# Performance work log

Hardware: AMD Instinct MI355X
Metric: run time of the kernel (lower is better)

The kernel has to match this reference:

```python
import jax, jax.numpy as jnp
import numpy as np

EPS = 1e-8

def elu_feature_map(x):
    return jax.nn.elu(x) + 1.0

def setup_inputs() -> dict:
    key = jax.random.key(0)
    ks = jax.random.split(key, 5)
    B, S, D = 2, 4096, 1024
    scale = 1.0 / np.sqrt(D).astype(np.float32)
    x = jax.random.normal(ks[0], (B, S, D), dtype=jnp.float32)
    Wq = jax.random.normal(ks[1], (D, D), dtype=jnp.float32) * scale
    Wk = jax.random.normal(ks[2], (D, D), dtype=jnp.float32) * scale
    Wv = jax.random.normal(ks[3], (D, D), dtype=jnp.float32) * scale
    Wo = jax.random.normal(ks[4], (D, D), dtype=jnp.float32) * scale
    return {"x": x, "Wq": Wq, "Wk": Wk, "Wv": Wv, "Wo": Wo}

def reference(x, Wq, Wk, Wv, Wo):
    B, S, D = x.shape
    H = 16
    Dh = D // H
    # projections (nn.Linear with no bias: x @ W.T)
    def proj(W):
        return (x @ W.T).reshape(B, S, H, Dh)
    q = elu_feature_map(proj(Wq))  # [B,S,H,Dh]
    k = elu_feature_map(proj(Wk))
    v = proj(Wv)
    # scan over sequence: carry running kv_sum [B,H,Dh,Dh] and k_sum [B,H,Dh]
    q_t = jnp.moveaxis(q, 1, 0)  # [S,B,H,Dh]
    k_t = jnp.moveaxis(k, 1, 0)
    v_t = jnp.moveaxis(v, 1, 0)

    def step(carry, qkv):
        kv_sum, k_sum = carry
        q_i, k_i, v_i = qkv  # each [B,H,Dh]
        kv_sum = kv_sum + jnp.einsum('bhd,bhe->bhde', k_i, v_i)
        k_sum = k_sum + k_i
        num = jnp.einsum('bhd,bhde->bhe', q_i, kv_sum)
        den = jnp.sum(q_i * k_sum, axis=-1, keepdims=True)
        out_i = num / (den + EPS)
        return (kv_sum, k_sum), out_i

    kv0 = jnp.zeros((B, H, Dh, Dh), dtype=x.dtype)
    ks0 = jnp.zeros((B, H, Dh), dtype=x.dtype)
    _, out = jax.lax.scan(step, (kv0, ks0), (q_t, k_t, v_t))  # out: [S,B,H,Dh]
    out = jnp.moveaxis(out, 0, 1).reshape(B, S, D)
    return out @ Wo.T
```

## Files before the change

kernel.cpp:

```cpp
#include <hip/hip_runtime.h>
#include <math.h>


#define EPSF 1e-8f

typedef unsigned short u16;
typedef unsigned int   u32;
typedef __attribute__((ext_vector_type(8))) short short8v;
typedef __attribute__((ext_vector_type(4))) float f32x4;

__device__ __forceinline__ float elu1(float x){ return x > 0.f ? x + 1.f : __expf(x); }
__device__ __forceinline__ u16 f2bf(float f){
    union{float f; u32 i;} c; c.f = f;
    u32 i = c.i + 0x7FFFu + ((c.i >> 16) & 1u);
    return (u16)(i >> 16);
}
__device__ __forceinline__ float bf2f(u16 v){ union{u32 i; float f;} c; c.i = (u32)v << 16; return c.f; }
__device__ __forceinline__ float bflo(u32 v){ union{u32 i; float f;} c; c.i = v << 16; return c.f; }
__device__ __forceinline__ float bfhi(u32 v){ union{u32 i; float f;} c; c.i = v & 0xffff0000u; return c.f; }
__device__ __forceinline__ void f4a(float4 v, float* a){ a[0]=v.x; a[1]=v.y; a[2]=v.z; a[3]=v.w; }

__device__ __forceinline__ void gload16(const void* g, void* l){
    __builtin_amdgcn_global_load_lds((const __attribute__((address_space(1))) u32*)g,
                                     (__attribute__((address_space(3))) u32*)l, 16, 0, 0);
}

__global__ __launch_bounds__(256) void k_cast5(
    const float* __restrict__ x,  const float* __restrict__ wq,
    const float* __restrict__ wk, const float* __restrict__ wv,
    const float* __restrict__ wo,
    u16* __restrict__ xb, u16* __restrict__ wcat, u16* __restrict__ wob)
{
    size_t i8 = ((size_t)blockIdx.x * 256 + threadIdx.x) * 8;
    const float* s; u16* d; size_t off;
    if      (i8 <  8388608) { s = x;  d = xb;            off = i8; }
    else if (i8 <  9437184) { s = wq; d = wcat;          off = i8 - 8388608; }
    else if (i8 < 10485760) { s = wk; d = wcat + 1048576; off = i8 - 9437184; }
    else if (i8 < 11534336) { s = wv; d = wcat + 2097152; off = i8 - 10485760; }
    else                    { s = wo; d = wob;           off = i8 - 11534336; }
    float4 a = *(const float4*)&s[off];
    float4 b = *(const float4*)&s[off + 4];
    uint4 p;
    p.x = (u32)f2bf(a.x) | ((u32)f2bf(a.y) << 16);
    p.y = (u32)f2bf(a.z) | ((u32)f2bf(a.w) << 16);
    p.z = (u32)f2bf(b.x) | ((u32)f2bf(b.y) << 16);
    p.w = (u32)f2bf(b.z) | ((u32)f2bf(b.w) << 16);
    *(uint4*)&d[off] = p;
}

__global__ __launch_bounds__(256, 3) void k_gemm6(
    const u16* __restrict__ Ag, const u16* __restrict__ Wg, u16* __restrict__ C)
{
    __shared__ __align__(16) char dsm[49152];
    const int bid = blockIdx.x;
    const int nid = (bid & 7) * 96 + (bid >> 3);
    const int bx  = nid / 24;
    const int by  = nid % 24;
    const int m0  = bx * 256;
    const int n0  = by * 128;

    const int tid = threadIdx.x;
    const int l   = tid & 63;
    const int wid = tid >> 6;
    const int wm  = wid >> 1;
    const int wn  = wid & 1;
    const int li  = l & 15;
    const int kgi = l >> 4;

    const int ra0 = wm*128 + li;
    const int offA0 = (ra0 >> 1)*128 + (((((ra0 & 1) << 2) | kgi) ^ ((ra0 >> 1) & 7)) << 4);
    const int rb0 = wn*64 + li;
    const int offB0 = (rb0 >> 1)*128 + (((((rb0 & 1) << 2) | kgi) ^ ((rb0 >> 1) & 7)) << 4);

    const int sx   = (l & 7) ^ (l >> 3);
    const int rowb = 2*(wid*8 + (l >> 3)) + (sx >> 2);
    const int skg  = (sx & 3) * 8;
    const u16* srcA = Ag + (size_t)(m0 + rowb) * 1024 + skg;
    const u16* srcB = Wg + (size_t)(n0 + rowb) * 1024 + skg;

    f32x4 acc[8][4];
    #pragma unroll
    for (int m = 0; m < 8; ++m)
        #pragma unroll
        for (int n = 0; n < 4; ++n) acc[m][n] = (f32x4){0.f, 0.f, 0.f, 0.f};

    #define ST6(BUF, T) { \
        char* ab = dsm + (BUF)*24576; \
        char* bb = dsm + (BUF)*24576 + 16384; \
        _Pragma("unroll") for (int j = 0; j < 4; ++j) \
            gload16(srcA + (size_t)j*65536 + (T)*32, ab + j*4096 + wid*1024); \
        _Pragma("unroll") for (int j = 0; j < 2; ++j) \
            gload16(srcB + (size_t)j*65536 + (T)*32, bb + j*4096 + wid*1024); }

    ST6(0, 0);
    asm volatile("s_waitcnt vmcnt(0)" ::: "memory");
    __builtin_amdgcn_s_barrier();

    #pragma unroll 1
    for (int t = 0; t < 32; ++t) {
        const int cur = t & 1;
        if (t < 31) ST6(cur ^ 1, t + 1);
        const char* Ab = dsm + cur*24576;
        const char* Bb = dsm + cur*24576 + 16384;
        short8v bfr[4];
        #pragma unroll
        for (int n = 0; n < 4; ++n) bfr[n] = *(const short8v*)(Bb + offB0 + n*1024);
        __builtin_amdgcn_s_setprio(1);
        #pragma unroll
        for (int m = 0; m < 8; ++m) {
            short8v afr = *(const short8v*)(Ab + offA0 + m*1024);
            #pragma unroll
            for (int n = 0; n < 4; ++n)
                acc[m][n] = __builtin_amdgcn_mfma_f32_16x16x32_bf16(afr, bfr[n], acc[m][n], 0, 0, 0);
        }
        __builtin_amdgcn_s_setprio(0);
        asm volatile("s_waitcnt vmcnt(0)" ::: "memory");
        __builtin_amdgcn_s_barrier();
    }
    #undef ST6

    const int matrix = by >> 3;
    const bool do_elu = matrix < 2;
    u16* outp = C + (size_t)matrix * 8388608;
    const int r0 = m0 + wm*128 + kgi*4;
    const int c0 = (by & 7)*128 + wn*64 + li;
    #pragma unroll
    for (int m = 0; m < 8; ++m)
        #pragma unroll
        for (int n = 0; n < 4; ++n)
            #pragma unroll
            for (int r = 0; r < 4; ++r) {
                float v = acc[m][n][r];
                if (do_elu) v = elu1(v);
                outp[(size_t)(r0 + m*16 + r) * 1024 + c0 + n*16] = f2bf(v);
            }
}

#define AOFF(BUF,KH) ((BUF)*49152 + (KH)*8192)
#define BOFF(BUF,KH) ((BUF)*49152 + 16384 + (KH)*16384)

#define ST(BUF, KT, KH) { \
    gload16(Ag + (size_t)(m0 + sRow)*1024 + (KT)*64 + (KH)*32 + sKg, dsm + AOFF(BUF,KH) + wvv*1024); \
    gload16(Wg + (size_t)(n0 + sRow)*1024 + (KT)*64 + (KH)*32 + sKg, dsm + BOFF(BUF,KH) + wvv*1024); \
    gload16(Wg + (size_t)(n0 + 128 + sRow)*1024 + (KT)*64 + (KH)*32 + sKg, dsm + BOFF(BUF,KH) + 8192 + wvv*1024); }

#define PH(BUF, KH, STCODE, CNT) { \
    short8v a[4], b[4]; \
    const char* Ab = dsm + AOFF(BUF,KH); \
    const char* Bb = dsm + BOFF(BUF,KH); \
    _Pragma("unroll") for (int m = 0; m < 4; ++m) a[m] = *(const short8v*)(Ab + offA[m]); \
    _Pragma("unroll") for (int n = 0; n < 4; ++n) b[n] = *(const short8v*)(Bb + offB[n]); \
    STCODE; \
    __builtin_amdgcn_s_setprio(1); \
    _Pragma("unroll") for (int m = 0; m < 4; ++m) \
        _Pragma("unroll") for (int n = 0; n < 4; ++n) \
            acc[m][n] = __builtin_amdgcn_mfma_f32_16x16x32_bf16(a[m], b[n], acc[m][n], 0, 0, 0); \
    __builtin_amdgcn_s_setprio(0); \
    asm volatile("s_waitcnt vmcnt(" #CNT ")" ::: "memory"); \
    __builtin_amdgcn_s_barrier(); }

template<int NBY>
__global__ __launch_bounds__(512, 2) void k_gemm5(
    const u16* __restrict__ Ag, const u16* __restrict__ Wg, float* __restrict__ Cv)
{
    extern __shared__ char dsm[];
    const int nid = (blockIdx.x & 7) * ((64 * NBY) >> 3) + (blockIdx.x >> 3);
    const int bx  = nid / NBY;
    const int by  = nid % NBY;
    const int m0  = bx * 128;
    const int n0  = by * 256;

    const int tid = threadIdx.x;
    const int l   = tid & 63;
    const int wid = tid >> 6;
    const int wm  = wid >> 2;
    const int wn  = wid & 3;
    const int li  = l & 15;
    const int kgi = l >> 4;

    int offA[4], offB[4];
    #pragma unroll
    for (int m = 0; m < 4; ++m) {
        int ra = wm*64 + m*16 + li;
        offA[m] = (ra >> 1)*128 + (((((ra & 1) << 2) | kgi) ^ ((ra >> 1) & 7)) << 4);
        int rb = wn*64 + m*16 + li;
        offB[m] = (rb >> 1)*128 + (((((rb & 1) << 2) | kgi) ^ ((rb >> 1) & 7)) << 4);
    }
    const int wvv  = wid;
    const int sx   = (l & 7) ^ (l >> 3);
    const int sRow = 2*(wvv*8 + (l >> 3)) + (sx >> 2);
    const int sKg  = (sx & 3) * 8;

    f32x4 acc[4][4];
    #pragma unroll
    for (int m = 0; m < 4; ++m)
        #pragma unroll
        for (int n = 0; n < 4; ++n) acc[m][n] = (f32x4){0.f, 0.f, 0.f, 0.f};

    ST(0, 0, 0); ST(0, 0, 1); ST(1, 1, 0);
    asm volatile("s_waitcnt vmcnt(6)" ::: "memory");
    __builtin_amdgcn_s_barrier();

    #pragma unroll 1
    for (int it = 0; it < 7; ++it) {
        const int T = it * 2;
        PH(0, 0, ST(1, T+1, 1), 6);
        PH(0, 1, ST(0, T+2, 0), 6);
        PH(1, 0, ST(0, T+2, 1), 6);
        PH(1, 1, ST(1, T+3, 0), 6);
    }
    PH(0, 0, ST(1, 15, 1), 6);
    PH(0, 1, {}, 3);
    PH(1, 0, {}, 0);
    {
        short8v a[4], b[4];
        const char* Ab = dsm + AOFF(1,1);
        const char* Bb = dsm + BOFF(1,1);
        #pragma unroll
        for (int m = 0; m < 4; ++m) a[m] = *(const short8v*)(Ab + offA[m]);
        #pragma unroll
        for (int n = 0; n < 4; ++n) b[n] = *(const short8v*)(Bb + offB[n]);
        #pragma unroll
        for (int m = 0; m < 4; ++m)
            #pragma unroll
            for (int n = 0; n < 4; ++n)
                acc[m][n] = __builtin_amdgcn_mfma_f32_16x16x32_bf16(a[m], b[n], acc[m][n], 0, 0, 0);
    }

    const int r0 = m0 + wm*64 + (l >> 4) * 4;
    const int c0 = n0 + wn*64 + li;
    #pragma unroll
    for (int m = 0; m < 4; ++m)
        #pragma unroll
        for (int n = 0; n < 4; ++n)
            #pragma unroll
            for (int r = 0; r < 4; ++r)
                Cv[(size_t)(r0 + m*16 + r) * 1024 + c0 + n*16] = acc[m][n][r];
}

__global__ __launch_bounds__(256) void k_chunksums(
    const u16* __restrict__ Kg, const u16* __restrict__ Vg,
    u16* __restrict__ CKVb, float* __restrict__ CKS)
{
    const int tid = threadIdx.x;
    const int tx = tid & 15, ty = tid >> 4;
    const int c  = blockIdx.x & 63;
    const int bh = blockIdx.x >> 6;
    const int b = bh >> 4, h = bh & 15;
    const int row0 = b * 4096 + c * 64;
    const int col  = h * 64;

    __shared__ float Ks[64][68];
    __shared__ float Vs[64][68];

    #pragma unroll
    for (int r = 0; r < 2; ++r) {
        int idx = tid + r * 256;
        int i = idx >> 3, cg = (idx & 7) << 3;
        uint4 ku = *(const uint4*)&Kg[(size_t)(row0 + i) * 1024 + col + cg];
        uint4 vu = *(const uint4*)&Vg[(size_t)(row0 + i) * 1024 + col + cg];
        Ks[i][cg+0]=bflo(ku.x); Ks[i][cg+1]=bfhi(ku.x);
        Ks[i][cg+2]=bflo(ku.y); Ks[i][cg+3]=bfhi(ku.y);
        Ks[i][cg+4]=bflo(ku.z); Ks[i][cg+5]=bfhi(ku.z);
        Ks[i][cg+6]=bflo(ku.w); Ks[i][cg+7]=bfhi(ku.w);
        Vs[i][cg+0]=bflo(vu.x); Vs[i][cg+1]=bfhi(vu.x);
        Vs[i][cg+2]=bflo(vu.y); Vs[i][cg+3]=bfhi(vu.y);
        Vs[i][cg+4]=bflo(vu.z); Vs[i][cg+5]=bfhi(vu.z);
        Vs[i][cg+6]=bflo(vu.w); Vs[i][cg+7]=bfhi(vu.w);
    }
    __syncthreads();

    float acc[4][4] = {};
    #pragma unroll 8
    for (int i = 0; i < 64; ++i) {
        float kv[4], vv[4];
        f4a(*(const float4*)&Ks[i][ty*4], kv);
        f4a(*(const float4*)&Vs[i][tx*4], vv);
        #pragma unroll
        for (int a = 0; a < 4; ++a)
            #pragma unroll
            for (int e = 0; e < 4; ++e)
                acc[a][e] = fmaf(kv[a], vv[e], acc[a][e]);
    }
    u16* ckv = &CKVb[(size_t)blockIdx.x * 4096];
    #pragma unroll
    for (int e = 0; e < 4; ++e) {
        u32 p0 = (u32)f2bf(acc[0][e]) | ((u32)f2bf(acc[1][e]) << 16);
        u32 p1 = (u32)f2bf(acc[2][e]) | ((u32)f2bf(acc[3][e]) << 16);
        *(uint2*)&ckv[(tx*4 + e) * 64 + ty*4] = make_uint2(p0, p1);
    }

    if (tid < 64) {
        float s = 0.f;
        #pragma unroll 8
        for (int i = 0; i < 64; ++i) s += Ks[i][tid];
        CKS[(size_t)blockIdx.x * 64 + tid] = s;
    }
}

__global__ __launch_bounds__(256) void k_prefix_kv(u16* __restrict__ CKV)
{
    const int bh = blockIdx.x >> 4;
    const int p  = ((blockIdx.x & 15) << 8) + threadIdx.x;
    const size_t base = (size_t)bh * 64 * 4096 + p;
    float acc = 0.f;
    #pragma unroll
    for (int c = 0; c < 64; ++c) {
        float t = bf2f(CKV[base + (size_t)c * 4096]);
        CKV[base + (size_t)c * 4096] = f2bf(acc);
        acc += t;
    }
}

__global__ __launch_bounds__(256) void k_prefix_ks(float* __restrict__ CKS)
{
    const int idx = blockIdx.x * 256 + threadIdx.x;
    const int bh = idx >> 6, d = idx & 63;
    const size_t base = (size_t)bh * 64 * 64 + d;
    float v[64];
    #pragma unroll
    for (int c = 0; c < 64; ++c) v[c] = CKS[base + (size_t)c * 64];
    float acc = 0.f;
    #pragma unroll
    for (int c = 0; c < 64; ++c) { float t = v[c]; CKS[base + (size_t)c * 64] = acc; acc += t; }
}

#define LSTR 72
__global__ __launch_bounds__(256) void k_attn2(
    const u16* __restrict__ Qg, const u16* __restrict__ Kg, const u16* __restrict__ Vg,
    const u16* __restrict__ Stg, const float* __restrict__ KSg, u16* __restrict__ AO)
{
    const int tid = threadIdx.x;
    const int l = tid & 63;
    const int w = tid >> 6;
    const int c  = blockIdx.x & 63;
    const int bh = blockIdx.x >> 6;
    const int row0 = (bh >> 4) * 4096 + c * 64;
    const int col  = (bh & 15) * 64;

    __shared__ __align__(16) u16 Qs [64 * LSTR];
    __shared__ __align__(16) u16 Ks [64 * LSTR];
    __shared__ __align__(16) u16 Vt [64 * LSTR];
    __shared__ __align__(16) u16 Sts[64 * LSTR];
    __shared__ __align__(16) u16 Pl [64 * LSTR];
    __shared__ float ksumF[64];
    __shared__ float invdenL[64];

    #pragma unroll
    for (int r = 0; r < 2; ++r) {
        int idx = tid + r * 256;
        int i = idx >> 3, cg = (idx & 7) << 3;
        *(uint4*)&Qs [i*LSTR + cg] = *(const uint4*)&Qg [(size_t)(row0 + i) * 1024 + col + cg];
        *(uint4*)&Ks [i*LSTR + cg] = *(const uint4*)&Kg [(size_t)(row0 + i) * 1024 + col + cg];
        *(uint4*)&Sts[i*LSTR + cg] = *(const uint4*)&Stg[(size_t)blockIdx.x * 4096 + i * 64 + cg];
        uint4 vu = *(const uint4*)&Vg[(size_t)(row0 + i) * 1024 + col + cg];
        Vt[(cg+0)*LSTR + i] = (u16)(vu.x & 0xffff);
        Vt[(cg+1)*LSTR + i] = (u16)(vu.x >> 16);
        Vt[(cg+2)*LSTR + i] = (u16)(vu.y & 0xffff);
        Vt[(cg+3)*LSTR + i] = (u16)(vu.y >> 16);
        Vt[(cg+4)*LSTR + i] = (u16)(vu.z & 0xffff);
        Vt[(cg+5)*LSTR + i] = (u16)(vu.z >> 16);
        Vt[(cg+6)*LSTR + i] = (u16)(vu.w & 0xffff);
        Vt[(cg+7)*LSTR + i] = (u16)(vu.w >> 16);
    }
    if (tid < 64) ksumF[tid] = KSg[(size_t)blockIdx.x * 64 + tid];
    __syncthreads();

    const int li = l & 15;
    const int lg = l >> 4;
    const int i_row = w * 16 + li;

    short8v bq[2];
    #pragma unroll
    for (int kc = 0; kc < 2; ++kc)
        bq[kc] = *(const short8v*)&Qs[i_row * LSTR + lg*8 + kc*32];

    float den = EPSF;
    #pragma unroll
    for (int mj = 0; mj < 4; ++mj) {
        f32x4 sacc = (f32x4){0.f, 0.f, 0.f, 0.f};
        #pragma unroll
        for (int kc = 0; kc < 2; ++kc) {
            short8v ak = *(const short8v*)&Ks[(mj*16 + li) * LSTR + lg*8 + kc*32];
            sacc = __builtin_amdgcn_mfma_f32_16x16x32_bf16(ak, bq[kc], sacc, 0, 0, 0);
        }
        const int jbase = mj*16 + lg*4;
        float pv[4];
        #pragma unroll
        for (int r = 0; r < 4; ++r) {
            float v = sacc[r];
            v = (jbase + r <= i_row) ? v : 0.f;
            den += v;
            pv[r] = v;
        }
        u32 lo = (u32)f2bf(pv[0]) | ((u32)f2bf(pv[1]) << 16);
        u32 hi = (u32)f2bf(pv[2]) | ((u32)f2bf(pv[3]) << 16);
        *(uint2*)&Pl[i_row * LSTR + jbase] = make_uint2(lo, hi);
    }

    {
        const int d0 = lg * 16;
        uint4 q1 = *(const uint4*)&Qs[i_row * LSTR + d0];
        uint4 q2 = *(const uint4*)&Qs[i_row * LSTR + d0 + 8];
        den += bflo(q1.x)*ksumF[d0+0] + bfhi(q1.x)*ksumF[d0+1]
             + bflo(q1.y)*ksumF[d0+2] + bfhi(q1.y)*ksumF[d0+3]
             + bflo(q1.z)*ksumF[d0+4] + bfhi(q1.z)*ksumF[d0+5]
             + bflo(q1.w)*ksumF[d0+6] + bfhi(q1.w)*ksumF[d0+7]
             + bflo(q2.x)*ksumF[d0+8] + bfhi(q2.x)*ksumF[d0+9]
             + bflo(q2.y)*ksumF[d0+10]+ bfhi(q2.y)*ksumF[d0+11]
             + bflo(q2.z)*ksumF[d0+12]+ bfhi(q2.z)*ksumF[d0+13]
             + bflo(q2.w)*ksumF[d0+14]+ bfhi(q2.w)*ksumF[d0+15];
    }
    den += __shfl_xor(den, 16);
    den += __shfl_xor(den, 32);
    if (l < 16) invdenL[w*16 + l] = 1.f / den;

    f32x4 oacc[4];
    #pragma unroll
    for (int ne = 0; ne < 4; ++ne) oacc[ne] = (f32x4){0.f, 0.f, 0.f, 0.f};
    #pragma unroll
    for (int kc = 0; kc < 2; ++kc) {
        short8v ap = *(const short8v*)&Pl[i_row * LSTR + lg*8 + kc*32];
        short8v aq = bq[kc];
        #pragma unroll
        for (int ne = 0; ne < 4; ++ne) {
            short8v bv = *(const short8v*)&Vt [(ne*16 + li) * LSTR + lg*8 + kc*32];
            short8v bs = *(const short8v*)&Sts[(ne*16 + li) * LSTR + lg*8 + kc*32];
            oacc[ne] = __builtin_amdgcn_mfma_f32_16x16x32_bf16(ap, bv, oacc[ne], 0, 0, 0);
            oacc[ne] = __builtin_amdgcn_mfma_f32_16x16x32_bf16(aq, bs, oacc[ne], 0, 0, 0);
        }
    }

    float inv[4];
    #pragma unroll
    for (int r = 0; r < 4; ++r) inv[r] = invdenL[w*16 + lg*4 + r];
    #pragma unroll
    for (int ne = 0; ne < 4; ++ne)
        #pragma unroll
        for (int r = 0; r < 4; ++r)
            Pl[(w*16 + lg*4 + r) * LSTR + ne*16 + li] = f2bf(oacc[ne][r] * inv[r]);

    #pragma unroll
    for (int p = 0; p < 2; ++p) {
        int idx2 = l + p * 64;
        int ro = w*16 + (idx2 >> 3), cg = (idx2 & 7) << 3;
        *(uint4*)&AO[(size_t)(row0 + ro) * 1024 + col + cg] = *(const uint4*)&Pl[ro*LSTR + cg];
    }
}

extern "C" void kernel_launch(void* const* d_in, const int* in_sizes, int n_in,
                              void* d_out, int out_size, void* d_ws, size_t ws_size,
                              hipStream_t stream)
{
    const float* x  = (const float*)d_in[0];
    const float* Wq = (const float*)d_in[1];
    const float* Wk = (const float*)d_in[2];
    const float* Wv = (const float*)d_in[3];
    const float* Wo = (const float*)d_in[4];
    float* out = (float*)d_out;

    char* w = (char*)d_ws;
    u16*   QKVb = (u16*)(w);
    u16*   Qb   = QKVb;
    u16*   Kb   = QKVb + 8388608;
    u16*   Vb   = QKVb + 16777216;
    u16*   xb   = (u16*)(w + 50331648);
    u16*   AOb  = xb;
    u16*   Wcat = (u16*)(w + 67108864);
    u16*   Wob  = (u16*)(w + 73400320);
    u16*   CKVb = (u16*)(w + 75497472);
    float* CKS  = (float*)(w + 92274688);

    hipFuncSetAttribute(reinterpret_cast<const void*>(k_gemm5<4>),
                        hipFuncAttributeMaxDynamicSharedMemorySize, 98304);

    k_cast5    <<<6144, 256, 0, stream>>>(x, Wq, Wk, Wv, Wo, xb, Wcat, Wob);
    k_gemm6    <<<768,  256, 0, stream>>>(xb, Wcat, QKVb);
    k_chunksums<<<2048, 256, 0, stream>>>(Kb, Vb, CKVb, CKS);
    k_prefix_kv<<<512,  256, 0, stream>>>(CKVb);
    k_prefix_ks<<<8,    256, 0, stream>>>(CKS);
    k_attn2    <<<2048, 256, 0, stream>>>(Qb, Kb, Vb, CKVb, CKS, AOb);
    k_gemm5<4> <<<256,  512, 98304, stream>>>(AOb, Wob, out);
}
```

Measured before the change: 140.6 us.

## Triple-buffer QKV GEMM, reuse it for output projection, merge prefix kernels

The QKV projection GEMM moves from double to triple buffering, so loads run two K-steps ahead and each step waits with a partial vmcnt instead of draining all loads. Occupancy drops from 3 to 2 blocks per CU because shared memory grows to 72KB. The same templated kernel, with an fp32 output mode, replaces the separate 512-thread output-projection GEMM, using 256x128 tiles and 256 blocks. The two prefix-sum kernels are merged into one launch to save a kernel launch.

```diff
diff --git a/kernel.cpp b/kernel.cpp
--- a/kernel.cpp
+++ b/kernel.cpp
@@ -48,14 +48,15 @@
     *(uint4*)&d[off] = p;
 }
 
-__global__ __launch_bounds__(256, 3) void k_gemm6(
-    const u16* __restrict__ Ag, const u16* __restrict__ Wg, u16* __restrict__ C)
-{
-    __shared__ __align__(16) char dsm[49152];
+template<int MODE, int NBY>
+__global__ __launch_bounds__(256, 2) void k_gemm7(
+    const u16* __restrict__ Ag, const u16* __restrict__ Wg, void* __restrict__ Cv)
+{
+    __shared__ __align__(16) char dsm[73728];
     const int bid = blockIdx.x;
-    const int nid = (bid & 7) * 96 + (bid >> 3);
-    const int bx  = nid / 24;
-    const int by  = nid % 24;
+    const int nid = (bid & 7) * ((32 * NBY) >> 3) + (bid >> 3);
+    const int bx  = nid / NBY;
+    const int by  = nid % NBY;
     const int m0  = bx * 256;
     const int n0  = by * 128;
 
@@ -84,158 +85,79 @@
         #pragma unroll
         for (int n = 0; n < 4; ++n) acc[m][n] = (f32x4){0.f, 0.f, 0.f, 0.f};
 
-    #define ST6(BUF, T) { \
+    #define ST7(BUF, T) { \
         char* ab = dsm + (BUF)*24576; \
-        char* bb = dsm + (BUF)*24576 + 16384; \
+        char* bb = ab + 16384; \
         _Pragma("unroll") for (int j = 0; j < 4; ++j) \
             gload16(srcA + (size_t)j*65536 + (T)*32, ab + j*4096 + wid*1024); \
         _Pragma("unroll") for (int j = 0; j < 2; ++j) \
             gload16(srcB + (size_t)j*65536 + (T)*32, bb + j*4096 + wid*1024); }
 
-    ST6(0, 0);
+    #define CP7(BUF) { \
+        const char* Ab = dsm + (BUF)*24576; \
+        const char* Bb = Ab + 16384; \
+        short8v bfr[4]; \
+        _Pragma("unroll") for (int n = 0; n < 4; ++n) bfr[n] = *(const short8v*)(Bb + offB0 + n*1024); \
+        __builtin_amdgcn_s_setprio(1); \
+        _Pragma("unroll") for (int m = 0; m < 8; ++m) { \
+            short8v afr = *(const short8v*)(Ab + offA0 + m*1024); \
+            _Pragma("unroll") for (int n = 0; n < 4; ++n) \
+                acc[m][n] = __builtin_amdgcn_mfma_f32_16x16x32_bf16(afr, bfr[n], acc[m][n], 0, 0, 0); \
+        } \
+        __builtin_amdgcn_s_setprio(0); }
+
+    #define STEP7(CUR, STB, TS) { \
+        ST7(STB, TS); \
+        CP7(CUR); \
+        asm volatile("s_waitcnt vmcnt(6)" ::: "memory"); \
+        __builtin_amdgcn_s_barrier(); }
+
+    ST7(0, 0); ST7(1, 1);
+    asm volatile("s_waitcnt vmcnt(6)" ::: "memory");
+    __builtin_amdgcn_s_barrier();
+
+    #pragma unroll 1
+    for (int g = 0; g < 10; ++g) {
+        const int t = g * 3;
+        STEP7(0, 2, t + 2);
+        STEP7(1, 0, t + 3);
+        STEP7(2, 1, t + 4);
+    }
+    CP7(0);
     asm volatile("s_waitcnt vmcnt(0)" ::: "memory");
     __builtin_amdgcn_s_barrier();
-
-    #pragma unroll 1
-    for (int t = 0; t < 32; ++t) {
-        const int cur = t & 1;
-        if (t < 31) ST6(cur ^ 1, t + 1);
-        const char* Ab = dsm + cur*24576;
-        const char* Bb = dsm + cur*24576 + 16384;
-        short8v bfr[4];
-        #pragma unroll
-        for (int n = 0; n < 4; ++n) bfr[n] = *(const short8v*)(Bb + offB0 + n*1024);
-        __builtin_amdgcn_s_setprio(1);
-        #pragma unroll
-        for (int m = 0; m < 8; ++m) {
-            short8v afr = *(const short8v*)(Ab + offA0 + m*1024);
+    CP7(1);
+    #undef STEP7
+    #undef CP7
+    #undef ST7
+
+    const int r0 = m0 + wm*128 + kgi*4;
+    if (MODE == 1) {
+        const int matrix = by >> 3;
+        const bool do_elu = matrix < 2;
+        u16* outp = (u16*)Cv + (size_t)matrix * 8388608;
+        const int c0 = (by & 7)*128 + wn*64 + li;
+        #pragma unroll
+        for (int m = 0; m < 8; ++m)
             #pragma unroll
             for (int n = 0; n < 4; ++n)
-                acc[m][n] = __builtin_amdgcn_mfma_f32_16x16x32_bf16(afr, bfr[n], acc[m][n], 0, 0, 0);
-        }
-        __builtin_amdgcn_s_setprio(0);
-        asm volatile("s_waitcnt vmcnt(0)" ::: "memory");
-        __builtin_amdgcn_s_barrier();
-    }
-    #undef ST6
-
-    const int matrix = by >> 3;
-    const bool do_elu = matrix < 2;
-    u16* outp = C + (size_t)matrix * 8388608;
-    const int r0 = m0 + wm*128 + kgi*4;
-    const int c0 = (by & 7)*128 + wn*64 + li;
-    #pragma unroll
-    for (int m = 0; m < 8; ++m)
-        #pragma unroll
-        for (int n = 0; n < 4; ++n)
-            #pragma unroll
-            for (int r = 0; r < 4; ++r) {
-                float v = acc[m][n][r];
-                if (do_elu) v = elu1(v);
-                outp[(size_t)(r0 + m*16 + r) * 1024 + c0 + n*16] = f2bf(v);
-            }
-}
-
-#define AOFF(BUF,KH) ((BUF)*49152 + (KH)*8192)
-#define BOFF(BUF,KH) ((BUF)*49152 + 16384 + (KH)*16384)
-
-#define ST(BUF, KT, KH) { \
-    gload16(Ag + (size_t)(m0 + sRow)*1024 + (KT)*64 + (KH)*32 + sKg, dsm + AOFF(BUF,KH) + wvv*1024); \
-    gload16(Wg + (size_t)(n0 + sRow)*1024 + (KT)*64 + (KH)*32 + sKg, dsm + BOFF(BUF,KH) + wvv*1024); \
-    gload16(Wg + (size_t)(n0 + 128 + sRow)*1024 + (KT)*64 + (KH)*32 + sKg, dsm + BOFF(BUF,KH) + 8192 + wvv*1024); }
-
-#define PH(BUF, KH, STCODE, CNT) { \
-    short8v a[4], b[4]; \
-    const char* Ab = dsm + AOFF(BUF,KH); \
-    const char* Bb = dsm + BOFF(BUF,KH); \
-    _Pragma("unroll") for (int m = 0; m < 4; ++m) a[m] = *(const short8v*)(Ab + offA[m]); \
-    _Pragma("unroll") for (int n = 0; n < 4; ++n) b[n] = *(const short8v*)(Bb + offB[n]); \
-    STCODE; \
-    __builtin_amdgcn_s_setprio(1); \
-    _Pragma("unroll") for (int m = 0; m < 4; ++m) \
-        _Pragma("unroll") for (int n = 0; n < 4; ++n) \
-            acc[m][n] = __builtin_amdgcn_mfma_f32_16x16x32_bf16(a[m], b[n], acc[m][n], 0, 0, 0); \
-    __builtin_amdgcn_s_setprio(0); \
-    asm volatile("s_waitcnt vmcnt(" #CNT ")" ::: "memory"); \
-    __builtin_amdgcn_s_barrier(); }
-
-template<int NBY>
-__global__ __launch_bounds__(512, 2) void k_gemm5(
-    const u16* __restrict__ Ag, const u16* __restrict__ Wg, float* __restrict__ Cv)
-{
-    extern __shared__ char dsm[];
-    const int nid = (blockIdx.x & 7) * ((64 * NBY) >> 3) + (blockIdx.x >> 3);
-    const int bx  = nid / NBY;
-    const int by  = nid % NBY;
-    const int m0  = bx * 128;
-    const int n0  = by * 256;
-
-    const int tid = threadIdx.x;
-    const int l   = tid & 63;
-    const int wid = tid >> 6;
-    const int wm  = wid >> 2;
-    const int wn  = wid & 3;
-    const int li  = l & 15;
-    const int kgi = l >> 4;
-
-    int offA[4], offB[4];
-    #pragma unroll
-    for (int m = 0; m < 4; ++m) {
-        int ra = wm*64 + m*16 + li;
-        offA[m] = (ra >> 1)*128 + (((((ra & 1) << 2) | kgi) ^ ((ra >> 1) & 7)) << 4);
-        int rb = wn*64 + m*16 + li;
-        offB[m] = (rb >> 1)*128 + (((((rb & 1) << 2) | kgi) ^ ((rb >> 1) & 7)) << 4);
-    }
-    const int wvv  = wid;
-    const int sx   = (l & 7) ^ (l >> 3);
-    const int sRow = 2*(wvv*8 + (l >> 3)) + (sx >> 2);
-    const int sKg  = (sx & 3) * 8;
-
-    f32x4 acc[4][4];
-    #pragma unroll
-    for (int m = 0; m < 4; ++m)
-        #pragma unroll
-        for (int n = 0; n < 4; ++n) acc[m][n] = (f32x4){0.f, 0.f, 0.f, 0.f};
-
-    ST(0, 0, 0); ST(0, 0, 1); ST(1, 1, 0);
-    asm volatile("s_waitcnt vmcnt(6)" ::: "memory");
-    __builtin_amdgcn_s_barrier();
-
-    #pragma unroll 1
-    for (int it = 0; it < 7; ++it) {
-        const int T = it * 2;
-        PH(0, 0, ST(1, T+1, 1), 6);
-        PH(0, 1, ST(0, T+2, 0), 6);
-        PH(1, 0, ST(0, T+2, 1), 6);
-        PH(1, 1, ST(1, T+3, 0), 6);
-    }
-    PH(0, 0, ST(1, 15, 1), 6);
-    PH(0, 1, {}, 3);
-    PH(1, 0, {}, 0);
-    {
-        short8v a[4], b[4];
-        const char* Ab = dsm + AOFF(1,1);
-        const char* Bb = dsm + BOFF(1,1);
-        #pragma unroll
-        for (int m = 0; m < 4; ++m) a[m] = *(const short8v*)(Ab + offA[m]);
-        #pragma unroll
-        for (int n = 0; n < 4; ++n) b[n] = *(const short8v*)(Bb + offB[n]);
-        #pragma unroll
-        for (int m = 0; m < 4; ++m)
+                #pragma unroll
+                for (int r = 0; r < 4; ++r) {
+                    float v = acc[m][n][r];
+                    if (do_elu) v = elu1(v);
+                    outp[(size_t)(r0 + m*16 + r) * 1024 + c0 + n*16] = f2bf(v);
+                }
+    } else {
+        float* outp = (float*)Cv;
+        const int c0 = by*128 + wn*64 + li;
+        #pragma unroll
+        for (int m = 0; m < 8; ++m)
             #pragma unroll
             for (int n = 0; n < 4; ++n)
-                acc[m][n] = __builtin_amdgcn_mfma_f32_16x16x32_bf16(a[m], b[n], acc[m][n], 0, 0, 0);
-    }
-
-    const int r0 = m0 + wm*64 + (l >> 4) * 4;
-    const int c0 = n0 + wn*64 + li;
-    #pragma unroll
-    for (int m = 0; m < 4; ++m)
-        #pragma unroll
-        for (int n = 0; n < 4; ++n)
-            #pragma unroll
-            for (int r = 0; r < 4; ++r)
-                Cv[(size_t)(r0 + m*16 + r) * 1024 + c0 + n*16] = acc[m][n][r];
+                #pragma unroll
+                for (int r = 0; r < 4; ++r)
+                    outp[(size_t)(r0 + m*16 + r) * 1024 + c0 + n*16] = acc[m][n][r];
+    }
 }
 
 __global__ __launch_bounds__(256) void k_chunksums(
@@ -298,31 +220,30 @@
     }
 }
 
-__global__ __launch_bounds__(256) void k_prefix_kv(u16* __restrict__ CKV)
-{
-    const int bh = blockIdx.x >> 4;
-    const int p  = ((blockIdx.x & 15) << 8) + threadIdx.x;
-    const size_t base = (size_t)bh * 64 * 4096 + p;
-    float acc = 0.f;
-    #pragma unroll
-    for (int c = 0; c < 64; ++c) {
-        float t = bf2f(CKV[base + (size_t)c * 4096]);
-        CKV[base + (size_t)c * 4096] = f2bf(acc);
-        acc += t;
-    }
-}
-
-__global__ __launch_bounds__(256) void k_prefix_ks(float* __restrict__ CKS)
-{
-    const int idx = blockIdx.x * 256 + threadIdx.x;
-    const int bh = idx >> 6, d = idx & 63;
-    const size_t base = (size_t)bh * 64 * 64 + d;
-    float v[64];
-    #pragma unroll
-    for (int c = 0; c < 64; ++c) v[c] = CKS[base + (size_t)c * 64];
-    float acc = 0.f;
-    #pragma unroll
-    for (int c = 0; c < 64; ++c) { float t = v[c]; CKS[base + (size_t)c * 64] = acc; acc += t; }
+__global__ __launch_bounds__(256) void k_prefix(u16* __restrict__ CKV, float* __restrict__ CKS)
+{
+    if (blockIdx.x < 512) {
+        const int bh = blockIdx.x >> 4;
+        const int p  = ((blockIdx.x & 15) << 8) + threadIdx.x;
+        const size_t base = (size_t)bh * 64 * 4096 + p;
+        float acc = 0.f;
+        #pragma unroll
+        for (int c = 0; c < 64; ++c) {
+            float t = bf2f(CKV[base + (size_t)c * 4096]);
+            CKV[base + (size_t)c * 4096] = f2bf(acc);
+            acc += t;
+        }
+    } else {
+        const int idx = (blockIdx.x - 512) * 256 + threadIdx.x;
+        const int bh = idx >> 6, d = idx & 63;
+        const size_t base = (size_t)bh * 64 * 64 + d;
+        float v[64];
+        #pragma unroll
+        for (int c = 0; c < 64; ++c) v[c] = CKS[base + (size_t)c * 64];
+        float acc = 0.f;
+        #pragma unroll
+        for (int c = 0; c < 64; ++c) { float t = v[c]; CKS[base + (size_t)c * 64] = acc; acc += t; }
+    }
 }
 
 #define LSTR 72
@@ -471,14 +392,10 @@
     u16*   CKVb = (u16*)(w + 75497472);
     float* CKS  = (float*)(w + 92274688);
 
-    hipFuncSetAttribute(reinterpret_cast<const void*>(k_gemm5<4>),
-                        hipFuncAttributeMaxDynamicSharedMemorySize, 98304);
-
-    k_cast5    <<<6144, 256, 0, stream>>>(x, Wq, Wk, Wv, Wo, xb, Wcat, Wob);
-    k_gemm6    <<<768,  256, 0, stream>>>(xb, Wcat, QKVb);
-    k_chunksums<<<2048, 256, 0, stream>>>(Kb, Vb, CKVb, CKS);
-    k_prefix_kv<<<512,  256, 0, stream>>>(CKVb);
-    k_prefix_ks<<<8,    256, 0, stream>>>(CKS);
-    k_attn2    <<<2048, 256, 0, stream>>>(Qb, Kb, Vb, CKVb, CKS, AOb);
-    k_gemm5<4> <<<256,  512, 98304, stream>>>(AOb, Wob, out);
-}
+    k_cast5       <<<6144, 256, 0, stream>>>(x, Wq, Wk, Wv, Wo, xb, Wcat, Wob);
+    k_gemm7<1,24> <<<768,  256, 0, stream>>>(xb, Wcat, (void*)QKVb);
+    k_chunksums   <<<2048, 256, 0, stream>>>(Kb, Vb, CKVb, CKS);
+    k_prefix      <<<520,  256, 0, stream>>>(CKVb, CKS);
+    k_attn2       <<<2048, 256, 0, stream>>>(Qb, Kb, Vb, CKVb, CKS, AOb);
+    k_gemm7<3,8>  <<<256,  256, 0, stream>>>(AOb, Wob, (void*)out);
+}
```

After: 140.4 us. About the same (-0.1%).
